# Optimization experiments

Hardware: AMD Instinct MI355X
Metric: run time of the kernel (lower is better)

The kernel has to match this reference:

```python
import jax, jax.numpy as jnp
import numpy as np
import math

DIM = 512
B, L = 32, 2048
NEG = jnp.float32(-2**32 + 1)  # padding value used by the torch module

def setup_inputs() -> dict:
    key = jax.random.key(0)
    k1, k2, k3, k4 = jax.random.split(key, 4)
    Ez = jax.random.normal(k1, (B, L, DIM), dtype=jnp.float32)
    # 6 Linear(dim, dim, bias=False) layers each for Q, K, V; weight is [out, in]
    s = 1.0 / math.sqrt(DIM)
    Wq = jax.random.uniform(k2, (6, DIM, DIM), dtype=jnp.float32, minval=-s, maxval=s)
    Wk = jax.random.uniform(k3, (6, DIM, DIM), dtype=jnp.float32, minval=-s, maxval=s)
    Wv = jax.random.uniform(k4, (6, DIM, DIM), dtype=jnp.float32, minval=-s, maxval=s)
    return {"Ez": Ez, "Wq": Wq, "Wk": Wk, "Wv": Wv, "z": 3}

def reference(Ez, Wq, Wk, Wv, z):
    dim = Ez.shape[-1]
    # nn.Linear: x @ W.T
    q = jnp.einsum('bld,ed->ble', Ez, Wq[z])
    k = jnp.einsum('bld,ed->ble', Ez, Wk[z])
    v = jnp.einsum('bld,ed->ble', Ez, Wv[z])
    scores = jnp.einsum('bqe,bke->bqk', q, k) / jnp.float32(math.sqrt(dim))
    Lq = scores.shape[-1]
    tril = jnp.tril(jnp.ones((Lq, Lq), dtype=jnp.float32))  # causal mask
    scores = jnp.where(tril[None, :, :] == 0, NEG, scores)
    attn = jax.nn.softmax(scores, axis=-1)
    return jnp.einsum('bqk,bke->bqe', attn, v)
```

## Files before the change

kernel.cpp:

```cpp
#include <hip/hip_runtime.h>
#include <hip/hip_bf16.h>


typedef __attribute__((ext_vector_type(8))) short short8;
typedef __attribute__((ext_vector_type(4))) short short4v;
typedef __attribute__((ext_vector_type(4))) float f32x4;

#define DIM 512
#define LSEQ 2048
#define NB 32
#define SCALE 0.04419417382415922f
#define LOG2E 1.4426950408889634f

__device__ __forceinline__ short f2bs(float f) {
  __hip_bfloat16 h = __float2bfloat16(f);
  return __builtin_bit_cast(short, h);
}

__device__ __forceinline__ void gld16(const void* g, void* l) {
  __builtin_amdgcn_global_load_lds(
      (const unsigned int __attribute__((address_space(1)))*)g,
      (unsigned int __attribute__((address_space(3)))*)l, 16, 0, 0);
}

__global__ __launch_bounds__(256) void wcvt_kernel(
    const float* __restrict__ Wq, const float* __restrict__ Wk,
    const float* __restrict__ Wv, const int* __restrict__ zp,
    short* __restrict__ Wb) {
  int z = *zp;
  int i = blockIdx.x * 256 + threadIdx.x;
  int g = i >> 15;
  int off = (i & 32767) * 8;
  int n = off >> 9, d0 = off & 511;
  int kt = d0 >> 5, c = d0 & 31;
  int sw = ((c >> 3) ^ ((n >> 1) & 3));
  const float* src = (g == 0 ? Wq : (g == 1 ? Wk : Wv)) + (size_t)z * DIM * DIM + off;
  float4 a = *(const float4*)src, b = *(const float4*)(src + 4);
  short8 v;
  v[0]=f2bs(a.x); v[1]=f2bs(a.y); v[2]=f2bs(a.z); v[3]=f2bs(a.w);
  v[4]=f2bs(b.x); v[5]=f2bs(b.y); v[6]=f2bs(b.z); v[7]=f2bs(b.w);
  *(short8*)&Wb[((size_t)(g * 16 + kt) * 512 + n) * 32 + sw * 8] = v;
}

__global__ __launch_bounds__(512, 4) void proj_kernel(
    const float* __restrict__ Ez, const short* __restrict__ Wb,
    short* __restrict__ Qb, short* __restrict__ Kb, short* __restrict__ Vtb) {
  int g = blockIdx.z;
  const short* W = Wb + (size_t)g * 16 * 512 * 32;
  __shared__ short As[2][64 * 32];
  __shared__ short Bs[2][512 * 32];
  int tid = threadIdx.x, lane = tid & 63, wid = tid >> 6;
  int l15 = lane & 15, lg = lane >> 4;
  int m0 = blockIdx.x * 64;
  int sw = (l15 >> 1) & 3;
  f32x4 zero4 = {0.f, 0.f, 0.f, 0.f};
  f32x4 acc[4][4];
  #pragma unroll
  for (int mi = 0; mi < 4; mi++)
    #pragma unroll
    for (int ni = 0; ni < 4; ni++) acc[mi][ni] = zero4;

  int arow = tid >> 3, aq = tid & 7;
  int aoff = arow * 32 + (((aq >> 1) ^ ((arow >> 1) & 3)) << 3) + (aq & 1) * 4;
  const float* aptr = Ez + (size_t)(m0 + arow) * DIM + aq * 4;

  {
    float4 a = *(const float4*)aptr;
    short4v av;
    av[0]=f2bs(a.x); av[1]=f2bs(a.y); av[2]=f2bs(a.z); av[3]=f2bs(a.w);
    *(short4v*)&As[0][aoff] = av;
    #pragma unroll
    for (int ii = 0; ii < 4; ii++) {
      int s = wid * 4 + ii;
      gld16(W + s * 512 + lane * 8, &Bs[0][s * 512]);
    }
  }
  __syncthreads();

  #pragma unroll 2
  for (int kt = 0; kt < 16; kt++) {
    int cur = kt & 1;
    float4 a;
    if (kt < 15) {
      a = *(const float4*)(aptr + (kt + 1) * 32);
      #pragma unroll
      for (int ii = 0; ii < 4; ii++) {
        int s = wid * 4 + ii;
        gld16(W + (size_t)(kt + 1) * 16384 + s * 512 + lane * 8, &Bs[cur ^ 1][s * 512]);
      }
    }
    short8 af[4], bf[4];
    #pragma unroll
    for (int mi = 0; mi < 4; mi++)
      af[mi] = *(const short8*)&As[cur][(mi * 16 + l15) * 32 + ((lg ^ sw) << 3)];
    #pragma unroll
    for (int ni = 0; ni < 4; ni++)
      bf[ni] = *(const short8*)&Bs[cur][(wid * 64 + ni * 16 + l15) * 32 + ((lg ^ sw) << 3)];
    __builtin_amdgcn_s_setprio(1);
    #pragma unroll
    for (int mi = 0; mi < 4; mi++)
      #pragma unroll
      for (int ni = 0; ni < 4; ni++)
        acc[mi][ni] = __builtin_amdgcn_mfma_f32_16x16x32_bf16(af[mi], bf[ni], acc[mi][ni], 0, 0, 0);
    __builtin_amdgcn_s_setprio(0);
    if (kt < 15) {
      short4v av;
      av[0]=f2bs(a.x); av[1]=f2bs(a.y); av[2]=f2bs(a.z); av[3]=f2bs(a.w);
      *(short4v*)&As[cur ^ 1][aoff] = av;
    }
    __syncthreads();
  }

  if (g == 2) {
    #pragma unroll
    for (int mi = 0; mi < 4; mi++) {
      int gm0 = m0 + mi * 16 + lg * 4;
      int b = gm0 >> 11, l0 = gm0 & (LSEQ - 1);
      int t = l0 >> 5, c0 = l0 & 31;
      #pragma unroll
      for (int ni = 0; ni < 4; ni++) {
        int e = wid * 64 + ni * 16 + l15;
        short4v v;
        v[0]=f2bs(acc[mi][ni][0]); v[1]=f2bs(acc[mi][ni][1]);
        v[2]=f2bs(acc[mi][ni][2]); v[3]=f2bs(acc[mi][ni][3]);
        size_t idx = ((size_t)(b * 64 + t) * 512 + e) * 32
                     + (((c0 >> 3) ^ ((e >> 1) & 3)) << 3) + (c0 & 7);
        *(short4v*)&Vtb[idx] = v;
      }
    }
  } else {
    short* dst = (g == 0 ? Qb : Kb);
    float sc = (g == 0 ? SCALE : 1.0f);
    #pragma unroll
    for (int mi = 0; mi < 4; mi++) {
      int gm0 = m0 + mi * 16 + lg * 4;
      #pragma unroll
      for (int ni = 0; ni < 4; ni++) {
        int gn = wid * 64 + ni * 16 + l15;
        #pragma unroll
        for (int r = 0; r < 4; r++)
          dst[(size_t)(gm0 + r) * DIM + gn] = f2bs(acc[mi][ni][r] * sc);
      }
    }
  }
}

__device__ __forceinline__ void stage_kv(const short* __restrict__ Kb,
                                         const short* __restrict__ Vtb,
                                         short* Klbuf, short* Vlbuf,
                                         int batch, int t, int wid, int lane) {
  #pragma unroll
  for (int ii = 0; ii < 4; ii++) {
    int r = wid + ii * 8;
    const short* src = Kb + (size_t)(batch * LSEQ + t * 32 + r) * DIM + ((lane ^ wid) * 8);
    gld16(src, Klbuf + r * 512);
  }
  const short* vt = Vtb + (size_t)(batch * 64 + t) * (512 * 32);
  #pragma unroll
  for (int ii = 0; ii < 4; ii++) {
    int s = wid * 4 + ii;
    gld16(vt + s * 512 + lane * 8, Vlbuf + s * 512);
  }
}

__global__ __launch_bounds__(512, 2) void attn_kernel(
    const short* __restrict__ Qb, const short* __restrict__ Kb,
    const short* __restrict__ Vtb, float* __restrict__ out) {
  __shared__ short Kl[2][32 * 512];
  __shared__ short Vl[2][512 * 32];
  __shared__ short P_lds[8][16][36];
  int tid = threadIdx.x, lane = tid & 63, wid = tid >> 6;
  int l15 = lane & 15, lg = lane >> 4;
  int batch = blockIdx.x;
  int sw3 = (l15 >> 1) & 3;
  f32x4 zero4 = {0.f, 0.f, 0.f, 0.f};
  short8 ones;
  #pragma unroll
  for (int i = 0; i < 8; i++) ones[i] = (short)0x3F80;

  for (int qpass = 0; qpass < 2; qpass++) {
    int qt = qpass ? (int)blockIdx.y : 15 - (int)blockIdx.y;
    int qb0 = qt * 128;
    int q0w = qb0 + wid * 16;
    int nt = qt * 4 + 4;

    stage_kv(Kb, Vtb, Kl[0], Vl[0], batch, 0, wid, lane);

    short8 qf[16];
    const short* qrow = Qb + (size_t)(batch * LSEQ + q0w + l15) * DIM;
    #pragma unroll
    for (int kt = 0; kt < 16; kt++) qf[kt] = *(const short8*)(qrow + kt * 32 + lg * 8);

    f32x4 oacc[32];
    #pragma unroll
    for (int i = 0; i < 32; i++) oacc[i] = zero4;
    f32x4 dacc = zero4;
    float mrun = -1e30f;

    __syncthreads();

    for (int t = 0; t < nt; t++) {
      int cur = t & 1;
      if (t + 1 < nt)
        stage_kv(Kb, Vtb, Kl[cur ^ 1], Vl[cur ^ 1], batch, t + 1, wid, lane);

      if (t * 32 <= q0w + 15) {
        const short* Kc = Kl[cur];
        const short* Vc = Vl[cur];
        f32x4 sacc[2] = {zero4, zero4};
        __builtin_amdgcn_s_setprio(1);
        #pragma unroll
        for (int kt = 0; kt < 16; kt++) {
          #pragma unroll
          for (int c = 0; c < 2; c++) {
            int kr = c * 16 + l15;
            int j = kt * 4 + lg;
            short8 bk = *(const short8*)&Kc[kr * 512 + ((j ^ (kr & 7)) * 8)];
            sacc[c] = __builtin_amdgcn_mfma_f32_16x16x32_bf16(qf[kt], bk, sacc[c], 0, 0, 0);
          }
        }
        __builtin_amdgcn_s_setprio(0);
        float s0[4], s1[4];
        float mx = -1e30f;
        #pragma unroll
        for (int r = 0; r < 4; r++) {
          int q = q0w + lg * 4 + r;
          s0[r] = sacc[0][r] * LOG2E;
          s1[r] = sacc[1][r] * LOG2E;
          if (t * 32 + l15 > q) s0[r] = -1e30f;
          if (t * 32 + 16 + l15 > q) s1[r] = -1e30f;
          mx = fmaxf(mx, fmaxf(s0[r], s1[r]));
        }
        #pragma unroll
        for (int off = 1; off < 64; off <<= 1) mx = fmaxf(mx, __shfl_xor(mx, off, 64));
        if (mx > mrun + 11.5f) {
          float alpha = exp2f(mrun - mx);
          mrun = mx;
          dacc[0] *= alpha; dacc[1] *= alpha; dacc[2] *= alpha; dacc[3] *= alpha;
          #pragma unroll
          for (int et = 0; et < 32; et++) {
            oacc[et][0] *= alpha; oacc[et][1] *= alpha;
            oacc[et][2] *= alpha; oacc[et][3] *= alpha;
          }
        }
        #pragma unroll
        for (int r = 0; r < 4; r++) {
          P_lds[wid][lg * 4 + r][l15] = f2bs(exp2f(s0[r] - mrun));
          P_lds[wid][lg * 4 + r][16 + l15] = f2bs(exp2f(s1[r] - mrun));
        }
        short8 pa = *(const short8*)&P_lds[wid][l15][lg * 8];
        __builtin_amdgcn_s_setprio(1);
        dacc = __builtin_amdgcn_mfma_f32_16x16x32_bf16(pa, ones, dacc, 0, 0, 0);
        #pragma unroll
        for (int et = 0; et < 32; et++) {
          short8 bv = *(const short8*)&Vc[(et * 16 + l15) * 32 + ((lg ^ sw3) * 8)];
          oacc[et] = __builtin_amdgcn_mfma_f32_16x16x32_bf16(pa, bv, oacc[et], 0, 0, 0);
        }
        __builtin_amdgcn_s_setprio(0);
      }
      __syncthreads();
    }
    float inv[4];
    #pragma unroll
    for (int r = 0; r < 4; r++) inv[r] = 1.0f / dacc[r];
    #pragma unroll
    for (int et = 0; et < 32; et++)
      #pragma unroll
      for (int r = 0; r < 4; r++) {
        int q = q0w + lg * 4 + r;
        out[((size_t)(batch * LSEQ + q)) * DIM + et * 16 + l15] = oacc[et][r] * inv[r];
      }
  }
}

extern "C" void kernel_launch(void* const* d_in, const int* in_sizes, int n_in,
                              void* d_out, int out_size, void* d_ws, size_t ws_size,
                              hipStream_t stream) {
  const float* Ez = (const float*)d_in[0];
  const float* Wq = (const float*)d_in[1];
  const float* Wk = (const float*)d_in[2];
  const float* Wv = (const float*)d_in[3];
  const int* zp = (const int*)d_in[4];
  float* out = (float*)d_out;
  short* Qb = (short*)d_ws;
  short* Kb = Qb + (size_t)NB * LSEQ * DIM;
  short* Vtb = Kb + (size_t)NB * LSEQ * DIM;
  short* Wb = (short*)d_out;
  hipLaunchKernelGGL(wcvt_kernel, dim3(384), dim3(256), 0, stream,
                     Wq, Wk, Wv, zp, Wb);
  hipLaunchKernelGGL(proj_kernel, dim3(1024, 1, 3), dim3(512), 0, stream,
                     Ez, Wb, Qb, Kb, Vtb);
  hipLaunchKernelGGL(attn_kernel, dim3(32, 8), dim3(512), 0, stream,
                     Qb, Kb, Vtb, out);
}
```

Baseline: 476.8 us.

## Split PV product across waves by output columns, sharing P through LDS

Result: slower. 574.0 us (+20.4%).

```diff
diff --git a/kernel.cpp b/kernel.cpp
--- a/kernel.cpp
+++ b/kernel.cpp
@@ -130,7 +130,7 @@
     }
   } else {
     short* dst = (g == 0 ? Qb : Kb);
-    float sc = (g == 0 ? SCALE : 1.0f);
+    float sc = (g == 0 ? SCALE * LOG2E : 1.0f);
     #pragma unroll
     for (int mi = 0; mi < 4; mi++) {
       int gm0 = m0 + mi * 16 + lg * 4;
@@ -168,11 +168,12 @@
     const short* __restrict__ Vtb, float* __restrict__ out) {
   __shared__ short Kl[2][32 * 512];
   __shared__ short Vl[2][512 * 32];
-  __shared__ short P_lds[8][16][36];
+  __shared__ short P_lds[128][36];
+  __shared__ float alpha_lds[8];
+  __shared__ float dsum[128];
   int tid = threadIdx.x, lane = tid & 63, wid = tid >> 6;
   int l15 = lane & 15, lg = lane >> 4;
   int batch = blockIdx.x;
-  int sw3 = (l15 >> 1) & 3;
   f32x4 zero4 = {0.f, 0.f, 0.f, 0.f};
   short8 ones;
   #pragma unroll
@@ -186,14 +187,16 @@
 
     stage_kv(Kb, Vtb, Kl[0], Vl[0], batch, 0, wid, lane);
 
-    short8 qf[16];
     const short* qrow = Qb + (size_t)(batch * LSEQ + q0w + l15) * DIM;
-    #pragma unroll
-    for (int kt = 0; kt < 16; kt++) qf[kt] = *(const short8*)(qrow + kt * 32 + lg * 8);
-
-    f32x4 oacc[32];
-    #pragma unroll
-    for (int i = 0; i < 32; i++) oacc[i] = zero4;
+    short8 qf[12];
+    #pragma unroll
+    for (int kt = 0; kt < 12; kt++) qf[kt] = *(const short8*)(qrow + kt * 32 + lg * 8);
+
+    f32x4 oacc[8][4];
+    #pragma unroll
+    for (int i = 0; i < 8; i++)
+      #pragma unroll
+      for (int j = 0; j < 4; j++) oacc[i][j] = zero4;
     f32x4 dacc = zero4;
     float mrun = -1e30f;
 
@@ -204,72 +207,111 @@
       if (t + 1 < nt)
         stage_kv(Kb, Vtb, Kl[cur ^ 1], Vl[cur ^ 1], batch, t + 1, wid, lane);
 
-      if (t * 32 <= q0w + 15) {
+      bool wave_active = (t * 32 <= q0w + 15);
+      float alpha_local = 1.f;
+      if (wave_active) {
+        short8 qs[4];
+        #pragma unroll
+        for (int j = 0; j < 4; j++)
+          qs[j] = *(const volatile short8*)(qrow + (12 + j) * 32 + lg * 8);
         const short* Kc = Kl[cur];
-        const short* Vc = Vl[cur];
         f32x4 sacc[2] = {zero4, zero4};
         __builtin_amdgcn_s_setprio(1);
         #pragma unroll
         for (int kt = 0; kt < 16; kt++) {
+          short8 qa = (kt < 12) ? qf[kt] : qs[kt - 12];
           #pragma unroll
           for (int c = 0; c < 2; c++) {
             int kr = c * 16 + l15;
             int j = kt * 4 + lg;
             short8 bk = *(const short8*)&Kc[kr * 512 + ((j ^ (kr & 7)) * 8)];
-            sacc[c] = __builtin_amdgcn_mfma_f32_16x16x32_bf16(qf[kt], bk, sacc[c], 0, 0, 0);
+            sacc[c] = __builtin_amdgcn_mfma_f32_16x16x32_bf16(qa, bk, sacc[c], 0, 0, 0);
           }
         }
         __builtin_amdgcn_s_setprio(0);
         float s0[4], s1[4];
         float mx = -1e30f;
+        bool diag = (t * 32 + 31 > q0w);
         #pragma unroll
         for (int r = 0; r < 4; r++) {
-          int q = q0w + lg * 4 + r;
-          s0[r] = sacc[0][r] * LOG2E;
-          s1[r] = sacc[1][r] * LOG2E;
-          if (t * 32 + l15 > q) s0[r] = -1e30f;
-          if (t * 32 + 16 + l15 > q) s1[r] = -1e30f;
+          s0[r] = sacc[0][r];
+          s1[r] = sacc[1][r];
+          if (diag) {
+            int q = q0w + lg * 4 + r;
+            if (t * 32 + l15 > q) s0[r] = -1e30f;
+            if (t * 32 + 16 + l15 > q) s1[r] = -1e30f;
+          }
           mx = fmaxf(mx, fmaxf(s0[r], s1[r]));
         }
         #pragma unroll
         for (int off = 1; off < 64; off <<= 1) mx = fmaxf(mx, __shfl_xor(mx, off, 64));
         if (mx > mrun + 11.5f) {
-          float alpha = exp2f(mrun - mx);
+          alpha_local = exp2f(mrun - mx);
           mrun = mx;
-          dacc[0] *= alpha; dacc[1] *= alpha; dacc[2] *= alpha; dacc[3] *= alpha;
-          #pragma unroll
-          for (int et = 0; et < 32; et++) {
-            oacc[et][0] *= alpha; oacc[et][1] *= alpha;
-            oacc[et][2] *= alpha; oacc[et][3] *= alpha;
+        }
+        #pragma unroll
+        for (int r = 0; r < 4; r++) {
+          P_lds[wid * 16 + lg * 4 + r][l15] = f2bs(exp2f(s0[r] - mrun));
+          P_lds[wid * 16 + lg * 4 + r][16 + l15] = f2bs(exp2f(s1[r] - mrun));
+        }
+        if (lane == 0) alpha_lds[wid] = alpha_local;
+      }
+      __syncthreads();
+      {
+        const short* Vc = Vl[cur];
+        short8 bv[4];
+        #pragma unroll
+        for (int e4 = 0; e4 < 4; e4++) {
+          int e = wid * 64 + e4 * 16 + l15;
+          bv[e4] = *(const short8*)&Vc[e * 32 + ((lg ^ ((l15 >> 1) & 3)) * 8)];
+        }
+        if (wave_active) {
+          if (alpha_local != 1.0f) {
+            dacc[0] *= alpha_local; dacc[1] *= alpha_local;
+            dacc[2] *= alpha_local; dacc[3] *= alpha_local;
           }
-        }
-        #pragma unroll
-        for (int r = 0; r < 4; r++) {
-          P_lds[wid][lg * 4 + r][l15] = f2bs(exp2f(s0[r] - mrun));
-          P_lds[wid][lg * 4 + r][16 + l15] = f2bs(exp2f(s1[r] - mrun));
-        }
-        short8 pa = *(const short8*)&P_lds[wid][l15][lg * 8];
+          short8 paw = *(const short8*)&P_lds[wid * 16 + l15][lg * 8];
+          dacc = __builtin_amdgcn_mfma_f32_16x16x32_bf16(paw, ones, dacc, 0, 0, 0);
+        }
         __builtin_amdgcn_s_setprio(1);
-        dacc = __builtin_amdgcn_mfma_f32_16x16x32_bf16(pa, ones, dacc, 0, 0, 0);
-        #pragma unroll
-        for (int et = 0; et < 32; et++) {
-          short8 bv = *(const short8*)&Vc[(et * 16 + l15) * 32 + ((lg ^ sw3) * 8)];
-          oacc[et] = __builtin_amdgcn_mfma_f32_16x16x32_bf16(pa, bv, oacc[et], 0, 0, 0);
+        #pragma unroll
+        for (int qt8 = 0; qt8 < 8; qt8++) {
+          if (t * 32 <= qb0 + qt8 * 16 + 15) {
+            float a = alpha_lds[qt8];
+            short8 pa = *(const short8*)&P_lds[qt8 * 16 + l15][lg * 8];
+            if (a != 1.0f) {
+              #pragma unroll
+              for (int e4 = 0; e4 < 4; e4++) {
+                oacc[qt8][e4][0] *= a; oacc[qt8][e4][1] *= a;
+                oacc[qt8][e4][2] *= a; oacc[qt8][e4][3] *= a;
+              }
+            }
+            #pragma unroll
+            for (int e4 = 0; e4 < 4; e4++)
+              oacc[qt8][e4] = __builtin_amdgcn_mfma_f32_16x16x32_bf16(pa, bv[e4], oacc[qt8][e4], 0, 0, 0);
+          }
         }
         __builtin_amdgcn_s_setprio(0);
       }
       __syncthreads();
     }
-    float inv[4];
-    #pragma unroll
-    for (int r = 0; r < 4; r++) inv[r] = 1.0f / dacc[r];
-    #pragma unroll
-    for (int et = 0; et < 32; et++)
+    if (l15 == 0) {
+      #pragma unroll
+      for (int r = 0; r < 4; r++) dsum[wid * 16 + lg * 4 + r] = dacc[r];
+    }
+    __syncthreads();
+    #pragma unroll
+    for (int qt8 = 0; qt8 < 8; qt8++) {
       #pragma unroll
       for (int r = 0; r < 4; r++) {
-        int q = q0w + lg * 4 + r;
-        out[((size_t)(batch * LSEQ + q)) * DIM + et * 16 + l15] = oacc[et][r] * inv[r];
-      }
+        float inv = 1.0f / dsum[qt8 * 16 + lg * 4 + r];
+        int q = qb0 + qt8 * 16 + lg * 4 + r;
+        #pragma unroll
+        for (int e4 = 0; e4 < 4; e4++)
+          out[((size_t)(batch * LSEQ + q)) * DIM + wid * 64 + e4 * 16 + l15] =
+              oacc[qt8][e4][r] * inv;
+      }
+    }
   }
 }
 
```
